# Kernel optimization log

Measured on AMD Instinct MI355X. Metric: run time of the kernel, lower is better.

Reference implementation:

```python
import jax, jax.numpy as jnp
import numpy as np

LAMBDA_MAX = 2.0  # standard re-scaled Laplacian assumption (DGL lambda_max=[2])
NUM_GRAPHS = 100


def _cheb(feat, src, dst, d_invsqrt, W, b):
    # DGL ChebConv: h = sum_i fc_i(X_i) + b, X_i = Chebyshev recursion on scaled Laplacian
    n = feat.shape[0]
    k = W.shape[0]
    re = 2.0 / LAMBDA_MAX

    def aggr(f):  # D^{-1/2} A D^{-1/2} f  via gather + segment_sum
        fh = f * d_invsqrt
        m = jax.ops.segment_sum(fh[src], dst, num_segments=n)
        return m * d_invsqrt

    X0 = feat
    h = X0 @ W[0]
    if k > 1:
        X1 = -re * aggr(X0) + X0 * (re - 1.0)
        h = h + X1 @ W[1]
        for i in range(2, k):
            Xi = -2.0 * re * aggr(X1) + X1 * (2.0 * (re - 1.0)) - X0
            h = h + Xi @ W[i]
            X0, X1 = X1, Xi
    return h + b


def _edgeconv(feat, src, dst, Wt, bt, Wp, bp):
    # DGL EdgeConv: out_i = max_{j->i} [theta(x_i - x_j) + phi(x_i)], 0 if no in-edges
    n = feat.shape[0]
    theta = (feat[dst] - feat[src]) @ Wt + bt           # [E, H]
    phi = feat @ Wp + bp                                # [N, H]
    msg = theta + phi[dst]                              # [E, H]
    agg = jax.ops.segment_max(msg, dst, num_segments=n)
    return jnp.where(jnp.isfinite(agg), agg, jnp.zeros((), feat.dtype))


def setup_inputs() -> dict:
    key = jax.random.key(0)
    ks = jax.random.split(key, 20)
    N, E, G = 100000, 1600000, NUM_GRAPHS
    IN, H, K = 16, 64, 3

    def lin(k, fan_in, shape):
        return jax.random.normal(k, shape, dtype=jnp.float32) * (1.0 / np.sqrt(fan_in))

    inp = {}
    inp["feat"] = jax.random.normal(ks[0], (N, IN), dtype=jnp.float32)
    inp["src"] = jax.random.randint(ks[1], (E,), 0, N)
    inp["dst"] = jax.random.randint(ks[2], (E,), 0, N)
    inp["graph_ids"] = jnp.sort(jax.random.randint(ks[3], (N,), 0, G))
    # ChebConv params: W [k, in, out], b [out]
    inp["W1"] = lin(ks[4], IN, (K, IN, H)); inp["b1"] = jnp.zeros((H,), jnp.float32)
    inp["W2"] = lin(ks[5], H, (K, H, H));   inp["b2"] = jnp.zeros((H,), jnp.float32)
    inp["W3"] = lin(ks[6], H, (K, H, H));   inp["b3"] = jnp.zeros((H,), jnp.float32)
    # EdgeConv params: theta + phi linears
    inp["Wt1"] = lin(ks[7], H, (H, H));  inp["bt1"] = jnp.zeros((H,), jnp.float32)
    inp["Wp1"] = lin(ks[8], H, (H, H));  inp["bp1"] = jnp.zeros((H,), jnp.float32)
    inp["Wt2"] = lin(ks[9], H, (H, H));  inp["bt2"] = jnp.zeros((H,), jnp.float32)
    inp["Wp2"] = lin(ks[10], H, (H, H)); inp["bp2"] = jnp.zeros((H,), jnp.float32)
    return inp


def reference(feat, src, dst, graph_ids, W1, b1, W2, b2, W3, b3,
              Wt1, bt1, Wp1, bp1, Wt2, bt2, Wp2, bp2):
    n = feat.shape[0]
    deg = jax.ops.segment_sum(jnp.ones((src.shape[0],), feat.dtype), dst, num_segments=n)
    d_invsqrt = (jnp.clip(deg, 1.0, None) ** -0.5)[:, None]  # [N, 1]

    h = jax.nn.relu(_cheb(feat, src, dst, d_invsqrt, W1, b1))
    h = jax.nn.relu(_edgeconv(h, src, dst, Wt1, bt1, Wp1, bp1))
    h = jax.nn.relu(_cheb(h, src, dst, d_invsqrt, W2, b2))
    h = jax.nn.relu(_edgeconv(h, src, dst, Wt2, bt2, Wp2, bp2))
    h = jax.nn.relu(_cheb(h, src, dst, d_invsqrt, W3, b3))

    # dgl.mean_nodes: per-graph mean pooling
    counts = jax.ops.segment_sum(jnp.ones((n,), h.dtype), graph_ids, num_segments=NUM_GRAPHS)
    hg = jax.ops.segment_sum(h, graph_ids, num_segments=NUM_GRAPHS)
    return hg / jnp.clip(counts, 1.0, None)[:, None]
```

## Files before the change

kernel.cpp:

```cpp
#include <hip/hip_runtime.h>
#include <hip/hip_bf16.h>
#include <math.h>

typedef __attribute__((ext_vector_type(8))) short short8;
typedef __attribute__((ext_vector_type(4))) float floatx4;

__device__ __forceinline__ unsigned short bfb(float x) {
    union { __hip_bfloat16 h; unsigned short u; } c;
    c.h = __float2bfloat16(x);
    return c.u;
}
__device__ __forceinline__ float bf2f(unsigned short u) {
    union { unsigned int i; float f; } c;
    c.i = ((unsigned int)u) << 16;
    return c.f;
}
__device__ __forceinline__ void acc2(float& lo, float& hi, unsigned d) {
    union { unsigned u; float f; } a, b;
    a.u = d << 16;
    b.u = d & 0xffff0000u;
    lo += a.f; hi += b.f;
}
__device__ __forceinline__ unsigned pkmaxu16(unsigned a, unsigned b) {
    unsigned d;
    asm("v_pk_max_u16 %0, %1, %2" : "=v"(d) : "v"(a), "v"(b));
    return d;
}


__global__ __launch_bounds__(256) void k_bhist(const int* __restrict__ dst, int* __restrict__ bcnt, int E) {
    __shared__ int h[512];
    int t = threadIdx.x;
    for (int i = t; i < 512; i += 256) h[i] = 0;
    __syncthreads();
    int step = gridDim.x * 256;
    for (int i = blockIdx.x * 256 + t; i < E; i += step) atomicAdd(&h[dst[i] >> 8], 1);
    __syncthreads();
    for (int i = t; i < 512; i += 256) if (h[i]) atomicAdd(&bcnt[i], h[i]);
}

__global__ __launch_bounds__(512) void k_scanBkt(const int* __restrict__ bcnt, int* __restrict__ boff,
                                                 int* __restrict__ bcur, int nb, int E) {
    __shared__ int s[512];
    int t = threadIdx.x;
    int v = (t < nb) ? bcnt[t] : 0;
    s[t] = v;
    __syncthreads();
    for (int off = 1; off < 512; off <<= 1) {
        int x = (t >= off) ? s[t - off] : 0;
        __syncthreads();
        s[t] += x;
        __syncthreads();
    }
    if (t < nb) { boff[t] = s[t] - v; bcur[t] = s[t] - v; }
    if (t == 0) boff[nb] = E;
}

#define PCHUNK 8192

__global__ __launch_bounds__(256) void k_partA(const int* __restrict__ src, const int* __restrict__ dst,
                                               int* __restrict__ bcur, unsigned* __restrict__ ebuf, int E) {
    __shared__ int h[512];
    __shared__ int base[512];
    int t = threadIdx.x;
    for (int i = t; i < 512; i += 256) h[i] = 0;
    __syncthreads();
    int start = blockIdx.x * PCHUNK;
    int end = start + PCHUNK < E ? start + PCHUNK : E;
    for (int i = start + t; i < end; i += 256) atomicAdd(&h[dst[i] >> 8], 1);
    __syncthreads();
    for (int i = t; i < 512; i += 256) {
        int c = h[i];
        base[i] = c ? atomicAdd(&bcur[i], c) : 0;
        h[i] = 0;
    }
    __syncthreads();
    for (int i = start + t; i < end; i += 256) {
        int d = dst[i];
        int b = d >> 8;
        int r = atomicAdd(&h[b], 1);
        ebuf[base[b] + r] = ((unsigned)src[i] << 8) | (unsigned)(d & 255);
    }
}

__global__ __launch_bounds__(256) void k_finish(const unsigned* __restrict__ ebuf, const int* __restrict__ boff,
                                                int* __restrict__ row_off, float* __restrict__ dinv,
                                                int* __restrict__ csr, int N, int E) {
    __shared__ int h[256];
    __shared__ int sc[256];
    __shared__ int cur[256];
    int b = blockIdx.x, t = threadIdx.x;
    h[t] = 0;
    __syncthreads();
    int beg = boff[b], end = boff[b + 1];
    for (int e = beg + t; e < end; e += 256) atomicAdd(&h[ebuf[e] & 255], 1);
    __syncthreads();
    int v = h[t];
    sc[t] = v;
    __syncthreads();
    for (int off = 1; off < 256; off <<= 1) {
        int x = (t >= off) ? sc[t - off] : 0;
        __syncthreads();
        sc[t] += x;
        __syncthreads();
    }
    int node = (b << 8) + t;
    int excl = beg + sc[t] - v;
    if (node < N) {
        row_off[node] = excl;
        dinv[node] = rsqrtf((float)(v > 1 ? v : 1));
    }
    cur[t] = excl;
    if (b == 0 && t == 0) row_off[N] = E;
    __syncthreads();
    for (int e = beg + t; e < end; e += 256) {
        unsigned ed = ebuf[e];
        int pos = atomicAdd(&cur[ed & 255], 1);
        csr[pos] = (int)(ed >> 8);
    }
}


__global__ __launch_bounds__(256) void k_feat16(const float* __restrict__ feat, const float* __restrict__ dinv,
                                                unsigned short* __restrict__ featd, int total) {
    int i = blockIdx.x * 256 + threadIdx.x;
    if (i < total) featd[i] = bfb(feat[i] * dinv[i >> 4]);
}


__global__ __launch_bounds__(256) void k_aggr16(const unsigned short* __restrict__ Xd, const float* __restrict__ Z,
                                                const float* __restrict__ dinv,
                                                const int* __restrict__ row_off, const int* __restrict__ csr,
                                                float* __restrict__ out, unsigned short* __restrict__ outd,
                                                float alpha, float beta, int zoff, int N) {
    int node = blockIdx.x * 4 + (threadIdx.x >> 6);
    if (node >= N) return;
    int lane = threadIdx.x & 63;
    int g = lane >> 2;
    int co = (lane & 3) * 8;
    int beg = row_off[node], end = row_off[node + 1];
    int deg = end - beg;
    int myOff = (lane < deg) ? (csr[beg + lane] << 5) : zoff;
    const char* base = (const char*)Xd + co;
    float a0 = 0.f, a1 = 0.f, a2 = 0.f, a3 = 0.f;
    {
        int o0 = __shfl(myOff, g);
        int o1 = __shfl(myOff, 16 + g);
        ushort4 x0 = *(const ushort4*)(base + o0);
        ushort4 x1 = *(const ushort4*)(base + o1);
        a0 += bf2f(x0.x); a1 += bf2f(x0.y); a2 += bf2f(x0.z); a3 += bf2f(x0.w);
        a0 += bf2f(x1.x); a1 += bf2f(x1.y); a2 += bf2f(x1.z); a3 += bf2f(x1.w);
    }
    if (deg > 32) {
        int dmain = deg < 64 ? deg : 64;
        for (int j = 32; j < dmain; j += 16) {
            int o = __shfl(myOff, j + g);
            ushort4 x = *(const ushort4*)(base + o);
            a0 += bf2f(x.x); a1 += bf2f(x.y); a2 += bf2f(x.z); a3 += bf2f(x.w);
        }
        for (int e = beg + 64; e < end; e += 16) {
            int idx = e + g;
            int s = csr[idx < end ? idx : end - 1];
            ushort4 x = *(const ushort4*)(base + (s << 5));
            if (idx < end) {
                a0 += bf2f(x.x); a1 += bf2f(x.y); a2 += bf2f(x.z); a3 += bf2f(x.w);
            }
        }
    }
    a0 += __shfl_xor(a0, 4); a0 += __shfl_xor(a0, 8); a0 += __shfl_xor(a0, 16); a0 += __shfl_xor(a0, 32);
    a1 += __shfl_xor(a1, 4); a1 += __shfl_xor(a1, 8); a1 += __shfl_xor(a1, 16); a1 += __shfl_xor(a1, 32);
    a2 += __shfl_xor(a2, 4); a2 += __shfl_xor(a2, 8); a2 += __shfl_xor(a2, 16); a2 += __shfl_xor(a2, 32);
    a3 += __shfl_xor(a3, 4); a3 += __shfl_xor(a3, 8); a3 += __shfl_xor(a3, 16); a3 += __shfl_xor(a3, 32);
    if (g == 0) {
        int c4 = (lane & 3) * 4;
        float dn = dinv[node];
        float v0 = alpha * dn * a0;
        float v1 = alpha * dn * a1;
        float v2 = alpha * dn * a2;
        float v3 = alpha * dn * a3;
        if (Z) {
            float4 zv = *(const float4*)&Z[(size_t)node * 16 + c4];
            v0 += beta * zv.x; v1 += beta * zv.y; v2 += beta * zv.z; v3 += beta * zv.w;
        }
        float4 r = { v0, v1, v2, v3 };
        *(float4*)&out[(size_t)node * 16 + c4] = r;
        if (outd) {
            ushort4 u = { bfb(v0 * dn), bfb(v1 * dn), bfb(v2 * dn), bfb(v3 * dn) };
            *(ushort4*)&outd[(size_t)node * 16 + c4] = u;
        }
    }
}


__global__ __launch_bounds__(256) void k_aggr64(const unsigned short* __restrict__ Xd,
                                                const unsigned short* __restrict__ Z,
                                                const float* __restrict__ dinv,
                                                const int* __restrict__ row_off, const int* __restrict__ csr,
                                                unsigned short* __restrict__ outb, unsigned short* __restrict__ outd,
                                                float alpha, float beta, int zoff, int N) {
    int node = blockIdx.x * 4 + (threadIdx.x >> 6);
    if (node >= N) return;
    int lane = threadIdx.x & 63;
    int g = lane >> 3;
    int co = (lane & 7) * 16;
    int beg = row_off[node], end = row_off[node + 1];
    int deg = end - beg;
    int myOff = (lane < deg) ? (csr[beg + lane] << 7) : zoff;
    const char* base = (const char*)Xd + co;
    float a0 = 0.f, a1 = 0.f, a2 = 0.f, a3 = 0.f, a4 = 0.f, a5 = 0.f, a6 = 0.f, a7 = 0.f;
    {
        int o0 = __shfl(myOff, g);
        int o1 = __shfl(myOff, 8 + g);
        int o2 = __shfl(myOff, 16 + g);
        int o3 = __shfl(myOff, 24 + g);
        uint4 x0 = *(const uint4*)(base + o0);
        uint4 x1 = *(const uint4*)(base + o1);
        uint4 x2 = *(const uint4*)(base + o2);
        uint4 x3 = *(const uint4*)(base + o3);
        acc2(a0, a1, x0.x); acc2(a2, a3, x0.y); acc2(a4, a5, x0.z); acc2(a6, a7, x0.w);
        acc2(a0, a1, x1.x); acc2(a2, a3, x1.y); acc2(a4, a5, x1.z); acc2(a6, a7, x1.w);
        acc2(a0, a1, x2.x); acc2(a2, a3, x2.y); acc2(a4, a5, x2.z); acc2(a6, a7, x2.w);
        acc2(a0, a1, x3.x); acc2(a2, a3, x3.y); acc2(a4, a5, x3.z); acc2(a6, a7, x3.w);
    }
    if (deg > 32) {
        int dmain = deg < 64 ? deg : 64;
        for (int j = 32; j < dmain; j += 8) {
            int o = __shfl(myOff, j + g);
            uint4 x = *(const uint4*)(base + o);
            acc2(a0, a1, x.x); acc2(a2, a3, x.y); acc2(a4, a5, x.z); acc2(a6, a7, x.w);
        }
        for (int e = beg + 64; e < end; e += 8) {
            int idx = e + g;
            int s = csr[idx < end ? idx : end - 1];
            uint4 x = *(const uint4*)(base + (s << 7));
            if (idx < end) {
                acc2(a0, a1, x.x); acc2(a2, a3, x.y); acc2(a4, a5, x.z); acc2(a6, a7, x.w);
            }
        }
    }
    a0 += __shfl_xor(a0, 8); a0 += __shfl_xor(a0, 16); a0 += __shfl_xor(a0, 32);
    a1 += __shfl_xor(a1, 8); a1 += __shfl_xor(a1, 16); a1 += __shfl_xor(a1, 32);
    a2 += __shfl_xor(a2, 8); a2 += __shfl_xor(a2, 16); a2 += __shfl_xor(a2, 32);
    a3 += __shfl_xor(a3, 8); a3 += __shfl_xor(a3, 16); a3 += __shfl_xor(a3, 32);
    a4 += __shfl_xor(a4, 8); a4 += __shfl_xor(a4, 16); a4 += __shfl_xor(a4, 32);
    a5 += __shfl_xor(a5, 8); a5 += __shfl_xor(a5, 16); a5 += __shfl_xor(a5, 32);
    a6 += __shfl_xor(a6, 8); a6 += __shfl_xor(a6, 16); a6 += __shfl_xor(a6, 32);
    a7 += __shfl_xor(a7, 8); a7 += __shfl_xor(a7, 16); a7 += __shfl_xor(a7, 32);
    if (g == 0) {
        float dn = dinv[node];
        float v[8] = { a0, a1, a2, a3, a4, a5, a6, a7 };
#pragma unroll
        for (int i = 0; i < 8; ++i) v[i] *= alpha * dn;
        size_t rb = (size_t)node * 128 + co;
        if (Z) {
            uint4 zv = *(const uint4*)((const char*)Z + rb);
            unsigned zd[4] = { zv.x, zv.y, zv.z, zv.w };
#pragma unroll
            for (int i = 0; i < 4; ++i) {
                union { unsigned u; float f; } lo, hi;
                lo.u = zd[i] << 16; hi.u = zd[i] & 0xffff0000u;
                v[2 * i] += beta * lo.f;
                v[2 * i + 1] += beta * hi.f;
            }
        }
        uint4 ub, ud;
        unsigned* pb = (unsigned*)&ub;
        unsigned* pd = (unsigned*)&ud;
#pragma unroll
        for (int i = 0; i < 4; ++i) {
            pb[i] = (unsigned)bfb(v[2 * i]) | ((unsigned)bfb(v[2 * i + 1]) << 16);
            pd[i] = (unsigned)bfb(v[2 * i] * dn) | ((unsigned)bfb(v[2 * i + 1] * dn) << 16);
        }
        *(uint4*)((char*)outb + rb) = ub;
        if (outd) *(uint4*)((char*)outd + rb) = ud;
    }
}


template <int KDIM, bool BIN16, bool BOUT16>
__global__ __launch_bounds__(256) void k_cheb_m(const void* __restrict__ X0v, const void* __restrict__ X1v,
                                                const void* __restrict__ X2v, const float* __restrict__ W,
                                                const float* __restrict__ b, void* __restrict__ outv, int N) {
    constexpr int KT = (KDIM == 16) ? 64 : 3 * KDIM;
    constexpr int SX = KT + 8;
    __shared__ unsigned short Xs[64 * SX];
    __shared__ unsigned short Ws[64 * SX];
    int t = threadIdx.x;

    {
        int sn = t & 63;
        int gn = blockIdx.x * 64 + sn; if (gn >= N) gn = N - 1;
        int k0 = (t >> 6) * (KDIM / 4);
        if constexpr (BIN16) {
            const unsigned short* Xp[3] = { (const unsigned short*)X0v, (const unsigned short*)X1v,
                                            (const unsigned short*)X2v };
#pragma unroll
            for (int a = 0; a < 3; ++a) {
#pragma unroll
                for (int i = 0; i < KDIM / 16; ++i) {
                    *(ushort4*)&Xs[sn * SX + a * KDIM + k0 + 4 * i] =
                        *(const ushort4*)&Xp[a][(size_t)gn * KDIM + k0 + 4 * i];
                }
            }
        } else {
            const float* Xp[3] = { (const float*)X0v, (const float*)X1v, (const float*)X2v };
#pragma unroll
            for (int a = 0; a < 3; ++a) {
#pragma unroll
                for (int i = 0; i < KDIM / 16; ++i) {
                    float4 v = *(const float4*)&Xp[a][(size_t)gn * KDIM + k0 + 4 * i];
                    ushort4 u = { bfb(v.x), bfb(v.y), bfb(v.z), bfb(v.w) };
                    *(ushort4*)&Xs[sn * SX + a * KDIM + k0 + 4 * i] = u;
                }
            }
        }
        if (KDIM == 16) {
            int kp = 48 + (t >> 6) * 4;
            ushort4 z = { 0, 0, 0, 0 };
            *(ushort4*)&Xs[sn * SX + kp] = z;
        }
    }
    for (int idx = t; idx < 3 * KDIM * 64; idx += 256) {
        int a = idx / (KDIM * 64);
        int r = idx % (KDIM * 64);
        int k = r >> 6, n = r & 63;
        Ws[n * SX + a * KDIM + k] = bfb(W[idx]);
    }
    if (KDIM == 16) {
        for (int idx = t; idx < 1024; idx += 256) {
            int n = idx & 63, k = 48 + (idx >> 6);
            Ws[n * SX + k] = 0;
        }
    }
    __syncthreads();

    int wave = t >> 6, lane = t & 63;
    int fi = lane & 15, quad = lane >> 4;
    int arow = wave * 16 + fi;

    floatx4 acc0 = {0.f,0.f,0.f,0.f}, acc1 = {0.f,0.f,0.f,0.f}, acc2v = {0.f,0.f,0.f,0.f}, acc3 = {0.f,0.f,0.f,0.f};
#pragma unroll
    for (int ks = 0; ks < KT / 32; ++ks) {
        short8 af = *(const short8*)&Xs[arow * SX + ks * 32 + quad * 8];
        short8 b0 = *(const short8*)&Ws[(0 * 16 + fi) * SX + ks * 32 + quad * 8];
        short8 b1 = *(const short8*)&Ws[(1 * 16 + fi) * SX + ks * 32 + quad * 8];
        short8 b2 = *(const short8*)&Ws[(2 * 16 + fi) * SX + ks * 32 + quad * 8];
        short8 b3 = *(const short8*)&Ws[(3 * 16 + fi) * SX + ks * 32 + quad * 8];
        acc0 = __builtin_amdgcn_mfma_f32_16x16x32_bf16(af, b0, acc0, 0, 0, 0);
        acc1 = __builtin_amdgcn_mfma_f32_16x16x32_bf16(af, b1, acc1, 0, 0, 0);
        acc2v = __builtin_amdgcn_mfma_f32_16x16x32_bf16(af, b2, acc2v, 0, 0, 0);
        acc3 = __builtin_amdgcn_mfma_f32_16x16x32_bf16(af, b3, acc3, 0, 0, 0);
    }

    int nbase = blockIdx.x * 64 + wave * 16 + quad * 4;
    floatx4 accs[4] = { acc0, acc1, acc2v, acc3 };
#pragma unroll
    for (int nt = 0; nt < 4; ++nt) {
        int col = nt * 16 + fi;
        float bias = b[col];
#pragma unroll
        for (int reg = 0; reg < 4; ++reg) {
            int node = nbase + reg;
            if (node < N) {
                float r = fmaxf(accs[nt][reg] + bias, 0.f);
                if constexpr (BOUT16) {
                    ((unsigned short*)outv)[(size_t)node * 64 + col] = bfb(r);
                } else {
                    ((float*)outv)[(size_t)node * 64 + col] = r;
                }
            }
        }
    }
}


__global__ __launch_bounds__(256) void k_e1_m(const unsigned short* X, const float* __restrict__ Wt,
                                              const float* __restrict__ Wp, const float* __restrict__ bt,
                                              const float* __restrict__ bp,
                                              unsigned short* md, float* __restrict__ pbuf, int N) {
    constexpr int SX = 72;
    __shared__ unsigned short Xs[64 * SX];
    __shared__ unsigned short Ws[128 * SX];
    int t = threadIdx.x;

    {
        int sn = t & 63;
        int gn = blockIdx.x * 64 + sn; if (gn >= N) gn = N - 1;
        int k0 = (t >> 6) * 16;
#pragma unroll
        for (int i = 0; i < 2; ++i) {
            *(short8*)&Xs[sn * SX + k0 + 8 * i] = *(const short8*)&X[(size_t)gn * 64 + k0 + 8 * i];
        }
    }
    for (int idx = t; idx < 4096; idx += 256) {
        int k = idx >> 6, n = idx & 63;
        float wt = Wt[idx];
        Ws[n * SX + k] = bfb(wt);
        Ws[(64 + n) * SX + k] = bfb(wt + Wp[idx]);
    }
    __syncthreads();

    int wave = t >> 6, lane = t & 63;
    int fi = lane & 15, quad = lane >> 4;
    int arow = wave * 16 + fi;

    floatx4 acc[8];
#pragma unroll
    for (int i = 0; i < 8; ++i) acc[i] = (floatx4){0.f,0.f,0.f,0.f};
#pragma unroll
    for (int ks = 0; ks < 2; ++ks) {
        short8 af = *(const short8*)&Xs[arow * SX + ks * 32 + quad * 8];
#pragma unroll
        for (int nt = 0; nt < 8; ++nt) {
            short8 bf = *(const short8*)&Ws[(nt * 16 + fi) * SX + ks * 32 + quad * 8];
            acc[nt] = __builtin_amdgcn_mfma_f32_16x16x32_bf16(af, bf, acc[nt], 0, 0, 0);
        }
    }

    int nbase = blockIdx.x * 64 + wave * 16 + quad * 4;
#pragma unroll
    for (int nt = 0; nt < 8; ++nt) {
        int col = nt * 16 + fi;
        if (col < 64) {
#pragma unroll
            for (int reg = 0; reg < 4; ++reg) {
                int node = nbase + reg;
                if (node < N) {
                    unsigned u = (unsigned)bfb(acc[nt][reg]) ^ 0x8000u;
                    unsigned key = (u & 0x8000u) ? (~u & 0xffffu) : (u | 0x8000u);
                    md[(size_t)node * 64 + col] = (unsigned short)key;
                }
            }
        } else {
            int cc = col - 64;
            float bias = bt[cc] + bp[cc];
#pragma unroll
            for (int reg = 0; reg < 4; ++reg) {
                int node = nbase + reg;
                if (node < N) pbuf[(size_t)node * 64 + cc] = acc[nt][reg] + bias;
            }
        }
    }
}


__global__ __launch_bounds__(256) void k_e2_b(const unsigned short* __restrict__ md, const float* __restrict__ pbuf,
                                              const int* __restrict__ row_off, const int* __restrict__ csr,
                                              const float* __restrict__ dinv, unsigned short* __restrict__ out,
                                              unsigned short* __restrict__ outd, int zoff, int N) {
    int node = blockIdx.x * 4 + (threadIdx.x >> 6);
    if (node >= N) return;
    int lane = threadIdx.x & 63;
    int g = lane >> 3;
    int co = (lane & 7) * 16;
    int beg = row_off[node], end = row_off[node + 1];
    int deg = end - beg;
    int dmain = deg < 64 ? deg : 64;
    int li = lane < dmain ? lane : dmain - 1;
    int myOff = (deg > 0) ? (csr[beg + li] << 7) : zoff;
    const char* base = (const char*)md + co;
    unsigned k0 = 0, k1 = 0, k2 = 0, k3 = 0;
    {
        int o0 = __shfl(myOff, g);
        int o1 = __shfl(myOff, 8 + g);
        int o2 = __shfl(myOff, 16 + g);
        int o3 = __shfl(myOff, 24 + g);
        uint4 x0 = *(const uint4*)(base + o0);
        uint4 x1 = *(const uint4*)(base + o1);
        uint4 x2 = *(const uint4*)(base + o2);
        uint4 x3 = *(const uint4*)(base + o3);
        k0 = pkmaxu16(k0, x0.x); k1 = pkmaxu16(k1, x0.y); k2 = pkmaxu16(k2, x0.z); k3 = pkmaxu16(k3, x0.w);
        k0 = pkmaxu16(k0, x1.x); k1 = pkmaxu16(k1, x1.y); k2 = pkmaxu16(k2, x1.z); k3 = pkmaxu16(k3, x1.w);
        k0 = pkmaxu16(k0, x2.x); k1 = pkmaxu16(k1, x2.y); k2 = pkmaxu16(k2, x2.z); k3 = pkmaxu16(k3, x2.w);
        k0 = pkmaxu16(k0, x3.x); k1 = pkmaxu16(k1, x3.y); k2 = pkmaxu16(k2, x3.z); k3 = pkmaxu16(k3, x3.w);
    }
    if (deg > 32) {
        for (int j = 32; j < dmain; j += 8) {
            int o = __shfl(myOff, j + g);
            uint4 x = *(const uint4*)(base + o);
            k0 = pkmaxu16(k0, x.x); k1 = pkmaxu16(k1, x.y); k2 = pkmaxu16(k2, x.z); k3 = pkmaxu16(k3, x.w);
        }
        for (int e = beg + 64; e < end; e += 8) {
            int idx = e + g;
            int s = csr[idx < end ? idx : end - 1];
            uint4 x = *(const uint4*)(base + (s << 7));
            k0 = pkmaxu16(k0, x.x); k1 = pkmaxu16(k1, x.y); k2 = pkmaxu16(k2, x.z); k3 = pkmaxu16(k3, x.w);
        }
    }
    k0 = pkmaxu16(k0, __shfl_xor((int)k0, 8)); k0 = pkmaxu16(k0, __shfl_xor((int)k0, 16)); k0 = pkmaxu16(k0, __shfl_xor((int)k0, 32));
    k1 = pkmaxu16(k1, __shfl_xor((int)k1, 8)); k1 = pkmaxu16(k1, __shfl_xor((int)k1, 16)); k1 = pkmaxu16(k1, __shfl_xor((int)k1, 32));
    k2 = pkmaxu16(k2, __shfl_xor((int)k2, 8)); k2 = pkmaxu16(k2, __shfl_xor((int)k2, 16)); k2 = pkmaxu16(k2, __shfl_xor((int)k2, 32));
    k3 = pkmaxu16(k3, __shfl_xor((int)k3, 8)); k3 = pkmaxu16(k3, __shfl_xor((int)k3, 16)); k3 = pkmaxu16(k3, __shfl_xor((int)k3, 32));
    if (g == 0) {
        unsigned kd[4] = { k0, k1, k2, k3 };
        float a[8];
#pragma unroll
        for (int i = 0; i < 4; ++i) {
            unsigned klo = kd[i] & 0xffffu, khi = kd[i] >> 16;
            unsigned short tlo = (klo & 0x8000u) ? (unsigned short)(klo & 0x7fffu) : (unsigned short)(~klo & 0xffffu);
            unsigned short thi = (khi & 0x8000u) ? (unsigned short)(khi & 0x7fffu) : (unsigned short)(~khi & 0xffffu);
            a[2 * i] = bf2f(tlo);
            a[2 * i + 1] = bf2f(thi);
        }
        float r[8];
        if (end > beg) {
            const float* pv = &pbuf[(size_t)node * 64 + (lane & 7) * 8];
            float4 p0 = *(const float4*)pv;
            float4 p1 = *(const float4*)(pv + 4);
            r[0] = fmaxf(p0.x + a[0], 0.f); r[1] = fmaxf(p0.y + a[1], 0.f);
            r[2] = fmaxf(p0.z + a[2], 0.f); r[3] = fmaxf(p0.w + a[3], 0.f);
            r[4] = fmaxf(p1.x + a[4], 0.f); r[5] = fmaxf(p1.y + a[5], 0.f);
            r[6] = fmaxf(p1.z + a[6], 0.f); r[7] = fmaxf(p1.w + a[7], 0.f);
        } else {
#pragma unroll
            for (int i = 0; i < 8; ++i) r[i] = 0.f;
        }
        float dn = dinv[node];
        size_t rb = (size_t)node * 128 + co;
        uint4 ub, ud;
        unsigned* pb = (unsigned*)&ub;
        unsigned* pd = (unsigned*)&ud;
#pragma unroll
        for (int i = 0; i < 4; ++i) {
            pb[i] = (unsigned)bfb(r[2 * i]) | ((unsigned)bfb(r[2 * i + 1]) << 16);
            pd[i] = (unsigned)bfb(r[2 * i] * dn) | ((unsigned)bfb(r[2 * i + 1] * dn) << 16);
        }
        *(uint4*)((char*)out + rb) = ub;
        *(uint4*)((char*)outd + rb) = ud;
    }
}


__global__ __launch_bounds__(256) void k_pool(const float* __restrict__ h, const int* __restrict__ gid,
                                              float* __restrict__ out, float* __restrict__ gcnt, int N) {
    const int CHUNK = 128;
    int wave = blockIdx.x * 4 + (threadIdx.x >> 6);
    int lane = threadIdx.x & 63;
    int beg = wave * CHUNK;
    if (beg >= N) return;
    int end = beg + CHUNK < N ? beg + CHUNK : N;
    int gcur = gid[beg];
    float acc = 0.f;
    int cnt = 0;
    for (int n = beg; n < end; ++n) {
        int g = gid[n];
        float v = h[n * 64 + lane];
        if (g != gcur) {
            atomicAdd(&out[gcur * 64 + lane], acc);
            if (lane == 0) atomicAdd(&gcnt[gcur], (float)cnt);
            gcur = g; acc = 0.f; cnt = 0;
        }
        acc += v;
        ++cnt;
    }
    atomicAdd(&out[gcur * 64 + lane], acc);
    if (lane == 0) atomicAdd(&gcnt[gcur], (float)cnt);
}

__global__ __launch_bounds__(256) void k_div(float* __restrict__ out, const float* __restrict__ gcnt, int total) {
    int i = blockIdx.x * blockDim.x + threadIdx.x;
    if (i < total) out[i] /= fmaxf(gcnt[i >> 6], 1.f);
}


extern "C" void kernel_launch(void* const* d_in, const int* in_sizes, int n_in,
                              void* d_out, int out_size, void* d_ws, size_t ws_size,
                              hipStream_t stream) {
    const float* feat = (const float*)d_in[0];
    const int* src = (const int*)d_in[1];
    const int* dst = (const int*)d_in[2];
    const int* gid = (const int*)d_in[3];
    const float* W1 = (const float*)d_in[4];  const float* b1 = (const float*)d_in[5];
    const float* W2 = (const float*)d_in[6];  const float* b2 = (const float*)d_in[7];
    const float* W3 = (const float*)d_in[8];  const float* b3 = (const float*)d_in[9];
    const float* Wt1 = (const float*)d_in[10]; const float* bt1 = (const float*)d_in[11];
    const float* Wp1 = (const float*)d_in[12]; const float* bp1 = (const float*)d_in[13];
    const float* Wt2 = (const float*)d_in[14]; const float* bt2 = (const float*)d_in[15];
    const float* Wp2 = (const float*)d_in[16]; const float* bp2 = (const float*)d_in[17];
    float* out = (float*)d_out;

    const int N = in_sizes[0] / 16;
    const int E = in_sizes[1];
    const int G = out_size / 64;
    const int nb = (N + 255) >> 8;

    char* p = (char*)d_ws;
    auto alloc = [&](size_t nbytes) {
        void* r = (void*)p;
        p += (nbytes + 255) & ~(size_t)255;
        return r;
    };
    int* row_off  = (int*)alloc((size_t)(N + 1) * 4);
    int* csr      = (int*)alloc((size_t)E * 4);
    int* bcnt     = (int*)alloc(512 * 4);
    int* boff     = (int*)alloc(513 * 4);
    int* bcur     = (int*)alloc(512 * 4);
    float* dinv   = (float*)alloc((size_t)N * 4);
    char* zpage   = (char*)alloc(256);
    float* bufA   = (float*)alloc((size_t)N * 64 * 4);
    float* bufB   = (float*)alloc((size_t)N * 64 * 4);
    float* bufC   = (float*)alloc((size_t)N * 64 * 4);
    float* bufD   = (float*)alloc((size_t)N * 64 * 4);
    unsigned short* md = (unsigned short*)alloc((size_t)N * 64 * 2);
    float* gcnt   = (float*)alloc((size_t)G * 4);

    unsigned* ebuf = (unsigned*)bufA;
    unsigned short* hd = (unsigned short*)bufC;
    unsigned short* xd = (unsigned short*)bufC + (size_t)N * 64;
    unsigned short* hb = md;
    unsigned short* hD = (unsigned short*)bufD;

    const int zo_hd = (int)((char*)zpage - (char*)hd);
    const int zo_xd = (int)((char*)zpage - (char*)xd);
    const int zo_md = (int)((char*)zpage - (char*)md);

    hipMemsetAsync(bcnt, 0, 512 * 4, stream);
    hipMemsetAsync(zpage, 0, 256, stream);
    hipMemsetAsync(gcnt, 0, (size_t)G * 4, stream);
    hipMemsetAsync(d_out, 0, (size_t)out_size * 4, stream);

    const int nb16 = (N * 16 + 255) / 256;
    const int nbw = (N + 3) / 4;
    const int npool = ((N + 127) / 128 + 3) / 4;
    const int nbt = (N + 63) / 64;
    const int npart = (E + PCHUNK - 1) / PCHUNK;

    k_bhist<<<256, 256, 0, stream>>>(dst, bcnt, E);
    k_scanBkt<<<1, 512, 0, stream>>>(bcnt, boff, bcur, nb, E);
    k_partA<<<npart, 256, 0, stream>>>(src, dst, bcur, ebuf, E);
    k_finish<<<nb, 256, 0, stream>>>(ebuf, boff, row_off, dinv, csr, N, E);

    k_feat16<<<nb16, 256, 0, stream>>>(feat, dinv, hd, N * 16);
    k_aggr16<<<nbw, 256, 0, stream>>>(hd, nullptr, dinv, row_off, csr, bufA, xd, -1.f, 0.f, zo_hd, N);
    k_aggr16<<<nbw, 256, 0, stream>>>(xd, feat, dinv, row_off, csr, bufB, nullptr, -2.f, -1.f, zo_xd, N);
    k_cheb_m<16, false, true><<<nbt, 256, 0, stream>>>(feat, bufA, bufB, W1, b1, hb, N);

    k_e1_m<<<nbt, 256, 0, stream>>>(hb, Wt1, Wp1, bt1, bp1, md, bufB, N);
    k_e2_b<<<nbw, 256, 0, stream>>>(md, bufB, row_off, csr, dinv, hD, hd, zo_md, N);

    k_aggr64<<<nbw, 256, 0, stream>>>(hd, nullptr, dinv, row_off, csr, (unsigned short*)bufA, xd, -1.f, 0.f, zo_hd, N);
    k_aggr64<<<nbw, 256, 0, stream>>>(xd, hD, dinv, row_off, csr, (unsigned short*)bufB, nullptr, -2.f, -1.f, zo_xd, N);
    k_cheb_m<64, true, true><<<nbt, 256, 0, stream>>>(hD, bufA, bufB, W2, b2, hb, N);

    k_e1_m<<<nbt, 256, 0, stream>>>(hb, Wt2, Wp2, bt2, bp2, md, bufB, N);
    k_e2_b<<<nbw, 256, 0, stream>>>(md, bufB, row_off, csr, dinv, hD, hd, zo_md, N);

    k_aggr64<<<nbw, 256, 0, stream>>>(hd, nullptr, dinv, row_off, csr, (unsigned short*)bufA, xd, -1.f, 0.f, zo_hd, N);
    k_aggr64<<<nbw, 256, 0, stream>>>(xd, hD, dinv, row_off, csr, (unsigned short*)bufB, nullptr, -2.f, -1.f, zo_xd, N);
    k_cheb_m<64, true, false><<<nbt, 256, 0, stream>>>(hD, bufA, bufB, W3, b3, bufC, N);

    k_pool<<<npool, 256, 0, stream>>>(bufC, gid, out, gcnt, N);
    k_div<<<(out_size + 255) / 256, 256, 0, stream>>>(out, gcnt, out_size);
}
```

Before: 595.2 us.

## Fuse EdgeConv linear into Cheb GEMM, reuse scaled aggregate, store phi in bf16

The separate EdgeConv node-linear kernel is folded into the Chebyshev GEMM epilogue, so the Cheb output goes through shared memory straight into the theta/phi MFMA. The first aggregation's plain output is no longer written; the Cheb kernel reads the D^-1/2-scaled copy and rescales its partial product by sqrt(deg). The phi buffer is stored as bf16 instead of fp32, and the three small memsets are merged into one. This removes a kernel launch and several full-size global writes and reads, in exchange for higher shared-memory and register use in the fused kernel and extra bf16 rounding on phi and the rescaled term.

New measurement: 568.3 us. 1.05x faster.

```diff
diff --git a/kernel.cpp b/kernel.cpp
--- a/kernel.cpp
+++ b/kernel.cpp
@@ -85,7 +85,7 @@
 
 __global__ __launch_bounds__(256) void k_finish(const unsigned* __restrict__ ebuf, const int* __restrict__ boff,
                                                 int* __restrict__ row_off, float* __restrict__ dinv,
-                                                int* __restrict__ csr, int N, int E) {
+                                                float* __restrict__ dsq, int* __restrict__ csr, int N, int E) {
     __shared__ int h[256];
     __shared__ int sc[256];
     __shared__ int cur[256];
@@ -108,7 +108,9 @@
     int excl = beg + sc[t] - v;
     if (node < N) {
         row_off[node] = excl;
-        dinv[node] = rsqrtf((float)(v > 1 ? v : 1));
+        float dg = (float)(v > 1 ? v : 1);
+        dinv[node] = rsqrtf(dg);
+        dsq[node] = sqrtf(dg);
     }
     cur[t] = excl;
     if (b == 0 && t == 0) row_off[N] = E;
@@ -263,28 +265,42 @@
                 v[2 * i + 1] += beta * hi.f;
             }
         }
-        uint4 ub, ud;
-        unsigned* pb = (unsigned*)&ub;
-        unsigned* pd = (unsigned*)&ud;
-#pragma unroll
-        for (int i = 0; i < 4; ++i) {
-            pb[i] = (unsigned)bfb(v[2 * i]) | ((unsigned)bfb(v[2 * i + 1]) << 16);
-            pd[i] = (unsigned)bfb(v[2 * i] * dn) | ((unsigned)bfb(v[2 * i + 1] * dn) << 16);
-        }
-        *(uint4*)((char*)outb + rb) = ub;
-        if (outd) *(uint4*)((char*)outd + rb) = ud;
-    }
-}
-
-
-template <int KDIM, bool BIN16, bool BOUT16>
-__global__ __launch_bounds__(256) void k_cheb_m(const void* __restrict__ X0v, const void* __restrict__ X1v,
-                                                const void* __restrict__ X2v, const float* __restrict__ W,
-                                                const float* __restrict__ b, void* __restrict__ outv, int N) {
+        if (outb) {
+            uint4 ub;
+            unsigned* pb = (unsigned*)&ub;
+#pragma unroll
+            for (int i = 0; i < 4; ++i)
+                pb[i] = (unsigned)bfb(v[2 * i]) | ((unsigned)bfb(v[2 * i + 1]) << 16);
+            *(uint4*)((char*)outb + rb) = ub;
+        }
+        if (outd) {
+            uint4 ud;
+            unsigned* pd = (unsigned*)&ud;
+#pragma unroll
+            for (int i = 0; i < 4; ++i)
+                pd[i] = (unsigned)bfb(v[2 * i] * dn) | ((unsigned)bfb(v[2 * i + 1] * dn) << 16);
+            *(uint4*)((char*)outd + rb) = ud;
+        }
+    }
+}
+
+
+template <int KDIM, bool BIN16, bool FUSE_E1>
+__global__ __launch_bounds__(256) void k_cheb(const void* __restrict__ X0v, const void* __restrict__ X1v,
+                                              const void* __restrict__ X2v, const float* __restrict__ dsq,
+                                              const float* __restrict__ W, const float* __restrict__ b,
+                                              const float* __restrict__ Wt, const float* __restrict__ Wp,
+                                              const float* __restrict__ bt, const float* __restrict__ bp,
+                                              unsigned short* __restrict__ md, unsigned short* __restrict__ pbuf,
+                                              float* __restrict__ outv, int N) {
     constexpr int KT = (KDIM == 16) ? 64 : 3 * KDIM;
     constexpr int SX = KT + 8;
-    __shared__ unsigned short Xs[64 * SX];
-    __shared__ unsigned short Ws[64 * SX];
+    constexpr int PH1 = 2 * 64 * SX;
+    constexpr int PH2 = FUSE_E1 ? (64 * 72 + 128 * 72) : 0;
+    constexpr int SSZ = PH1 > PH2 ? PH1 : PH2;
+    __shared__ unsigned short S[SSZ];
+    unsigned short* Xs = S;
+    unsigned short* Ws = S + 64 * SX;
     int t = threadIdx.x;
 
     {
@@ -314,7 +330,7 @@
                 }
             }
         }
-        if (KDIM == 16) {
+        if constexpr (KDIM == 16) {
             int kp = 48 + (t >> 6) * 4;
             ushort4 z = { 0, 0, 0, 0 };
             *(ushort4*)&Xs[sn * SX + kp] = z;
@@ -326,7 +342,7 @@
         int k = r >> 6, n = r & 63;
         Ws[n * SX + a * KDIM + k] = bfb(W[idx]);
     }
-    if (KDIM == 16) {
+    if constexpr (KDIM == 16) {
         for (int idx = t; idx < 1024; idx += 256) {
             int n = idx & 63, k = 48 + (idx >> 6);
             Ws[n * SX + k] = 0;
@@ -338,113 +354,123 @@
     int fi = lane & 15, quad = lane >> 4;
     int arow = wave * 16 + fi;
 
-    floatx4 acc0 = {0.f,0.f,0.f,0.f}, acc1 = {0.f,0.f,0.f,0.f}, acc2v = {0.f,0.f,0.f,0.f}, acc3 = {0.f,0.f,0.f,0.f};
+    floatx4 accA[4], accM[4];
+#pragma unroll
+    for (int i = 0; i < 4; ++i) { accA[i] = (floatx4){0.f,0.f,0.f,0.f}; accM[i] = (floatx4){0.f,0.f,0.f,0.f}; }
 #pragma unroll
     for (int ks = 0; ks < KT / 32; ++ks) {
+        constexpr bool hasMid = BIN16 && (KDIM == 64);
         short8 af = *(const short8*)&Xs[arow * SX + ks * 32 + quad * 8];
         short8 b0 = *(const short8*)&Ws[(0 * 16 + fi) * SX + ks * 32 + quad * 8];
         short8 b1 = *(const short8*)&Ws[(1 * 16 + fi) * SX + ks * 32 + quad * 8];
         short8 b2 = *(const short8*)&Ws[(2 * 16 + fi) * SX + ks * 32 + quad * 8];
         short8 b3 = *(const short8*)&Ws[(3 * 16 + fi) * SX + ks * 32 + quad * 8];
-        acc0 = __builtin_amdgcn_mfma_f32_16x16x32_bf16(af, b0, acc0, 0, 0, 0);
-        acc1 = __builtin_amdgcn_mfma_f32_16x16x32_bf16(af, b1, acc1, 0, 0, 0);
-        acc2v = __builtin_amdgcn_mfma_f32_16x16x32_bf16(af, b2, acc2v, 0, 0, 0);
-        acc3 = __builtin_amdgcn_mfma_f32_16x16x32_bf16(af, b3, acc3, 0, 0, 0);
+        if (hasMid && ks >= 2 && ks < 4) {
+            accM[0] = __builtin_amdgcn_mfma_f32_16x16x32_bf16(af, b0, accM[0], 0, 0, 0);
+            accM[1] = __builtin_amdgcn_mfma_f32_16x16x32_bf16(af, b1, accM[1], 0, 0, 0);
+            accM[2] = __builtin_amdgcn_mfma_f32_16x16x32_bf16(af, b2, accM[2], 0, 0, 0);
+            accM[3] = __builtin_amdgcn_mfma_f32_16x16x32_bf16(af, b3, accM[3], 0, 0, 0);
+        } else {
+            accA[0] = __builtin_amdgcn_mfma_f32_16x16x32_bf16(af, b0, accA[0], 0, 0, 0);
+            accA[1] = __builtin_amdgcn_mfma_f32_16x16x32_bf16(af, b1, accA[1], 0, 0, 0);
+            accA[2] = __builtin_amdgcn_mfma_f32_16x16x32_bf16(af, b2, accA[2], 0, 0, 0);
+            accA[3] = __builtin_amdgcn_mfma_f32_16x16x32_bf16(af, b3, accA[3], 0, 0, 0);
+        }
     }
 
     int nbase = blockIdx.x * 64 + wave * 16 + quad * 4;
-    floatx4 accs[4] = { acc0, acc1, acc2v, acc3 };
+    float dd[4];
+#pragma unroll
+    for (int reg = 0; reg < 4; ++reg) {
+        if constexpr (BIN16 && KDIM == 64) {
+            int node = nbase + reg;
+            dd[reg] = dsq[node < N ? node : N - 1];
+        } else dd[reg] = 0.f;
+    }
+    float rv[4][4];
 #pragma unroll
     for (int nt = 0; nt < 4; ++nt) {
         int col = nt * 16 + fi;
         float bias = b[col];
 #pragma unroll
         for (int reg = 0; reg < 4; ++reg) {
-            int node = nbase + reg;
-            if (node < N) {
-                float r = fmaxf(accs[nt][reg] + bias, 0.f);
-                if constexpr (BOUT16) {
-                    ((unsigned short*)outv)[(size_t)node * 64 + col] = bfb(r);
-                } else {
-                    ((float*)outv)[(size_t)node * 64 + col] = r;
-                }
-            }
-        }
-    }
-}
-
-
-__global__ __launch_bounds__(256) void k_e1_m(const unsigned short* X, const float* __restrict__ Wt,
-                                              const float* __restrict__ Wp, const float* __restrict__ bt,
-                                              const float* __restrict__ bp,
-                                              unsigned short* md, float* __restrict__ pbuf, int N) {
-    constexpr int SX = 72;
-    __shared__ unsigned short Xs[64 * SX];
-    __shared__ unsigned short Ws[128 * SX];
-    int t = threadIdx.x;
-
-    {
-        int sn = t & 63;
-        int gn = blockIdx.x * 64 + sn; if (gn >= N) gn = N - 1;
-        int k0 = (t >> 6) * 16;
-#pragma unroll
-        for (int i = 0; i < 2; ++i) {
-            *(short8*)&Xs[sn * SX + k0 + 8 * i] = *(const short8*)&X[(size_t)gn * 64 + k0 + 8 * i];
-        }
-    }
-    for (int idx = t; idx < 4096; idx += 256) {
-        int k = idx >> 6, n = idx & 63;
-        float wt = Wt[idx];
-        Ws[n * SX + k] = bfb(wt);
-        Ws[(64 + n) * SX + k] = bfb(wt + Wp[idx]);
-    }
-    __syncthreads();
-
-    int wave = t >> 6, lane = t & 63;
-    int fi = lane & 15, quad = lane >> 4;
-    int arow = wave * 16 + fi;
-
-    floatx4 acc[8];
-#pragma unroll
-    for (int i = 0; i < 8; ++i) acc[i] = (floatx4){0.f,0.f,0.f,0.f};
-#pragma unroll
-    for (int ks = 0; ks < 2; ++ks) {
-        short8 af = *(const short8*)&Xs[arow * SX + ks * 32 + quad * 8];
-#pragma unroll
-        for (int nt = 0; nt < 8; ++nt) {
-            short8 bf = *(const short8*)&Ws[(nt * 16 + fi) * SX + ks * 32 + quad * 8];
-            acc[nt] = __builtin_amdgcn_mfma_f32_16x16x32_bf16(af, bf, acc[nt], 0, 0, 0);
-        }
-    }
-
-    int nbase = blockIdx.x * 64 + wave * 16 + quad * 4;
-#pragma unroll
-    for (int nt = 0; nt < 8; ++nt) {
-        int col = nt * 16 + fi;
-        if (col < 64) {
+            float v = accA[nt][reg] + bias;
+            if constexpr (BIN16 && KDIM == 64) v += accM[nt][reg] * dd[reg];
+            rv[nt][reg] = fmaxf(v, 0.f);
+        }
+    }
+
+    if constexpr (!FUSE_E1) {
+#pragma unroll
+        for (int nt = 0; nt < 4; ++nt) {
+            int col = nt * 16 + fi;
 #pragma unroll
             for (int reg = 0; reg < 4; ++reg) {
                 int node = nbase + reg;
-                if (node < N) {
-                    unsigned u = (unsigned)bfb(acc[nt][reg]) ^ 0x8000u;
-                    unsigned key = (u & 0x8000u) ? (~u & 0xffffu) : (u | 0x8000u);
-                    md[(size_t)node * 64 + col] = (unsigned short)key;
+                if (node < N) outv[(size_t)node * 64 + col] = rv[nt][reg];
+            }
+        }
+    } else {
+        __syncthreads();
+        unsigned short* Hs = S;
+        unsigned short* W2 = S + 64 * 72;
+        int lrow = wave * 16 + quad * 4;
+#pragma unroll
+        for (int nt = 0; nt < 4; ++nt) {
+#pragma unroll
+            for (int reg = 0; reg < 4; ++reg) {
+                Hs[(lrow + reg) * 72 + nt * 16 + fi] = bfb(rv[nt][reg]);
+            }
+        }
+        for (int idx = t; idx < 4096; idx += 256) {
+            int k = idx >> 6, n = idx & 63;
+            float wt = Wt[idx];
+            W2[n * 72 + k] = bfb(wt);
+            W2[(64 + n) * 72 + k] = bfb(wt + Wp[idx]);
+        }
+        __syncthreads();
+
+        floatx4 ae[8];
+#pragma unroll
+        for (int i = 0; i < 8; ++i) ae[i] = (floatx4){0.f,0.f,0.f,0.f};
+#pragma unroll
+        for (int ks = 0; ks < 2; ++ks) {
+            short8 af = *(const short8*)&Hs[arow * 72 + ks * 32 + quad * 8];
+#pragma unroll
+            for (int nt = 0; nt < 8; ++nt) {
+                short8 bf = *(const short8*)&W2[(nt * 16 + fi) * 72 + ks * 32 + quad * 8];
+                ae[nt] = __builtin_amdgcn_mfma_f32_16x16x32_bf16(af, bf, ae[nt], 0, 0, 0);
+            }
+        }
+#pragma unroll
+        for (int nt = 0; nt < 8; ++nt) {
+            int col = nt * 16 + fi;
+            if (col < 64) {
+#pragma unroll
+                for (int reg = 0; reg < 4; ++reg) {
+                    int node = nbase + reg;
+                    if (node < N) {
+                        unsigned u = (unsigned)bfb(ae[nt][reg]) ^ 0x8000u;
+                        unsigned key = (u & 0x8000u) ? (~u & 0xffffu) : (u | 0x8000u);
+                        md[(size_t)node * 64 + col] = (unsigned short)key;
+                    }
                 }
-            }
-        } else {
-            int cc = col - 64;
-            float bias = bt[cc] + bp[cc];
-#pragma unroll
-            for (int reg = 0; reg < 4; ++reg) {
-                int node = nbase + reg;
-                if (node < N) pbuf[(size_t)node * 64 + cc] = acc[nt][reg] + bias;
-            }
-        }
-    }
-}
-
-
-__global__ __launch_bounds__(256) void k_e2_b(const unsigned short* __restrict__ md, const float* __restrict__ pbuf,
+            } else {
+                int cc = col - 64;
+                float bias = bt[cc] + bp[cc];
+#pragma unroll
+                for (int reg = 0; reg < 4; ++reg) {
+                    int node = nbase + reg;
+                    if (node < N) pbuf[(size_t)node * 64 + cc] = bfb(ae[nt][reg] + bias);
+                }
+            }
+        }
+    }
+}
+
+
+__global__ __launch_bounds__(256) void k_e2_b(const unsigned short* __restrict__ md,
+                                              const unsigned short* __restrict__ pbuf,
                                               const int* __restrict__ row_off, const int* __restrict__ csr,
                                               const float* __restrict__ dinv, unsigned short* __restrict__ out,
                                               unsigned short* __restrict__ outd, int zoff, int N) {
@@ -504,13 +530,13 @@
         }
         float r[8];
         if (end > beg) {
-            const float* pv = &pbuf[(size_t)node * 64 + (lane & 7) * 8];
-            float4 p0 = *(const float4*)pv;
-            float4 p1 = *(const float4*)(pv + 4);
-            r[0] = fmaxf(p0.x + a[0], 0.f); r[1] = fmaxf(p0.y + a[1], 0.f);
-            r[2] = fmaxf(p0.z + a[2], 0.f); r[3] = fmaxf(p0.w + a[3], 0.f);
-            r[4] = fmaxf(p1.x + a[4], 0.f); r[5] = fmaxf(p1.y + a[5], 0.f);
-            r[6] = fmaxf(p1.z + a[6], 0.f); r[7] = fmaxf(p1.w + a[7], 0.f);
+            uint4 pk = *(const uint4*)((const char*)pbuf + (size_t)node * 128 + co);
+            unsigned pd4[4] = { pk.x, pk.y, pk.z, pk.w };
+#pragma unroll
+            for (int i = 0; i < 4; ++i) {
+                r[2 * i]     = fmaxf(bf2f((unsigned short)(pd4[i] & 0xffffu)) + a[2 * i], 0.f);
+                r[2 * i + 1] = fmaxf(bf2f((unsigned short)(pd4[i] >> 16)) + a[2 * i + 1], 0.f);
+            }
         } else {
 #pragma unroll
             for (int i = 0; i < 8; ++i) r[i] = 0.f;
@@ -590,33 +616,36 @@
         p += (nbytes + 255) & ~(size_t)255;
         return r;
     };
+    int* bcnt     = (int*)alloc(512 * 4);
+    char* zpage   = (char*)alloc(256);
+    float* gcnt   = (float*)alloc((size_t)G * 4);
+    size_t zspan  = (size_t)((char*)gcnt - (char*)bcnt) + (((size_t)G * 4 + 255) & ~(size_t)255);
+    int* boff     = (int*)alloc(513 * 4);
+    int* bcur     = (int*)alloc(512 * 4);
     int* row_off  = (int*)alloc((size_t)(N + 1) * 4);
     int* csr      = (int*)alloc((size_t)E * 4);
-    int* bcnt     = (int*)alloc(512 * 4);
-    int* boff     = (int*)alloc(513 * 4);
-    int* bcur     = (int*)alloc(512 * 4);
     float* dinv   = (float*)alloc((size_t)N * 4);
-    char* zpage   = (char*)alloc(256);
+    float* dsq    = (float*)alloc((size_t)N * 4);
     float* bufA   = (float*)alloc((size_t)N * 64 * 4);
     float* bufB   = (float*)alloc((size_t)N * 64 * 4);
     float* bufC   = (float*)alloc((size_t)N * 64 * 4);
     float* bufD   = (float*)alloc((size_t)N * 64 * 4);
-    unsigned short* md = (unsigned short*)alloc((size_t)N * 64 * 2);
-    float* gcnt   = (float*)alloc((size_t)G * 4);
+    unsigned short* md   = (unsigned short*)alloc((size_t)N * 64 * 2);
+    unsigned short* pbuf = (unsigned short*)alloc((size_t)N * 64 * 2);
 
     unsigned* ebuf = (unsigned*)bufA;
     unsigned short* hd = (unsigned short*)bufC;
-    unsigned short* xd = (unsigned short*)bufC + (size_t)N * 64;
-    unsigned short* hb = md;
+    unsigned short* xd = hd + (size_t)N * 64;
+    unsigned short* xd3 = (unsigned short*)bufA;
     unsigned short* hD = (unsigned short*)bufD;
+    unsigned short* bufB16 = (unsigned short*)bufB;
 
     const int zo_hd = (int)((char*)zpage - (char*)hd);
     const int zo_xd = (int)((char*)zpage - (char*)xd);
+    const int zo_xd3 = (int)((char*)zpage - (char*)xd3);
     const int zo_md = (int)((char*)zpage - (char*)md);
 
-    hipMemsetAsync(bcnt, 0, 512 * 4, stream);
-    hipMemsetAsync(zpage, 0, 256, stream);
-    hipMemsetAsync(gcnt, 0, (size_t)G * 4, stream);
+    hipMemsetAsync(bcnt, 0, zspan, stream);
     hipMemsetAsync(d_out, 0, (size_t)out_size * 4, stream);
 
     const int nb16 = (N * 16 + 255) / 256;
@@ -628,26 +657,26 @@
     k_bhist<<<256, 256, 0, stream>>>(dst, bcnt, E);
     k_scanBkt<<<1, 512, 0, stream>>>(bcnt, boff, bcur, nb, E);
     k_partA<<<npart, 256, 0, stream>>>(src, dst, bcur, ebuf, E);
-    k_finish<<<nb, 256, 0, stream>>>(ebuf, boff, row_off, dinv, csr, N, E);
+    k_finish<<<nb, 256, 0, stream>>>(ebuf, boff, row_off, dinv, dsq, csr, N, E);
 
     k_feat16<<<nb16, 256, 0, stream>>>(feat, dinv, hd, N * 16);
     k_aggr16<<<nbw, 256, 0, stream>>>(hd, nullptr, dinv, row_off, csr, bufA, xd, -1.f, 0.f, zo_hd, N);
     k_aggr16<<<nbw, 256, 0, stream>>>(xd, feat, dinv, row_off, csr, bufB, nullptr, -2.f, -1.f, zo_xd, N);
-    k_cheb_m<16, false, true><<<nbt, 256, 0, stream>>>(feat, bufA, bufB, W1, b1, hb, N);
-
-    k_e1_m<<<nbt, 256, 0, stream>>>(hb, Wt1, Wp1, bt1, bp1, md, bufB, N);
-    k_e2_b<<<nbw, 256, 0, stream>>>(md, bufB, row_off, csr, dinv, hD, hd, zo_md, N);
-
-    k_aggr64<<<nbw, 256, 0, stream>>>(hd, nullptr, dinv, row_off, csr, (unsigned short*)bufA, xd, -1.f, 0.f, zo_hd, N);
-    k_aggr64<<<nbw, 256, 0, stream>>>(xd, hD, dinv, row_off, csr, (unsigned short*)bufB, nullptr, -2.f, -1.f, zo_xd, N);
-    k_cheb_m<64, true, true><<<nbt, 256, 0, stream>>>(hD, bufA, bufB, W2, b2, hb, N);
-
-    k_e1_m<<<nbt, 256, 0, stream>>>(hb, Wt2, Wp2, bt2, bp2, md, bufB, N);
-    k_e2_b<<<nbw, 256, 0, stream>>>(md, bufB, row_off, csr, dinv, hD, hd, zo_md, N);
-
-    k_aggr64<<<nbw, 256, 0, stream>>>(hd, nullptr, dinv, row_off, csr, (unsigned short*)bufA, xd, -1.f, 0.f, zo_hd, N);
-    k_aggr64<<<nbw, 256, 0, stream>>>(xd, hD, dinv, row_off, csr, (unsigned short*)bufB, nullptr, -2.f, -1.f, zo_xd, N);
-    k_cheb_m<64, true, false><<<nbt, 256, 0, stream>>>(hD, bufA, bufB, W3, b3, bufC, N);
+    k_cheb<16, false, true><<<nbt, 256, 0, stream>>>(feat, bufA, bufB, nullptr, W1, b1,
+                                                     Wt1, Wp1, bt1, bp1, md, pbuf, nullptr, N);
+    k_e2_b<<<nbw, 256, 0, stream>>>(md, pbuf, row_off, csr, dinv, hD, hd, zo_md, N);
+
+    k_aggr64<<<nbw, 256, 0, stream>>>(hd, nullptr, dinv, row_off, csr, nullptr, xd, -1.f, 0.f, zo_hd, N);
+    k_aggr64<<<nbw, 256, 0, stream>>>(xd, hD, dinv, row_off, csr, bufB16, nullptr, -2.f, -1.f, zo_xd, N);
+    k_cheb<64, true, true><<<nbt, 256, 0, stream>>>(hD, xd, bufB16, dsq, W2, b2,
+                                                    Wt2, Wp2, bt2, bp2, md, pbuf, nullptr, N);
+    k_e2_b<<<nbw, 256, 0, stream>>>(md, pbuf, row_off, csr, dinv, hD, hd, zo_md, N);
+
+    k_aggr64<<<nbw, 256, 0, stream>>>(hd, nullptr, dinv, row_off, csr, nullptr, xd3, -1.f, 0.f, zo_hd, N);
+    k_aggr64<<<nbw, 256, 0, stream>>>(xd3, hD, dinv, row_off, csr, bufB16, nullptr, -2.f, -1.f, zo_xd3, N);
+    k_cheb<64, true, false><<<nbt, 256, 0, stream>>>(hD, xd3, bufB16, dsq, W3, b3,
+                                                     nullptr, nullptr, nullptr, nullptr,
+                                                     nullptr, nullptr, bufC, N);
 
     k_pool<<<npool, 256, 0, stream>>>(bufC, gid, out, gcnt, N);
     k_div<<<(out_size + 255) / 256, 256, 0, stream>>>(out, gcnt, out_size);
```
